# Optimization experiments

Hardware: AMD Instinct MI355X
Metric: run time of the kernel (lower is better)

Reference implementation:

```python
import jax, jax.numpy as jnp
import numpy as np

B, S, IN_F, OUT_F, R = 4, 4096, 4096, 4096, 1024  # new_r = sqrt((4096+4096)*128) = 1024


def setup_inputs() -> dict:
    key = jax.random.key(0)
    kx, kw, kb, ka = jax.random.split(key, 4)
    x = jax.random.normal(kx, (B, S, IN_F), dtype=jnp.float32)
    W = jax.random.normal(kw, (OUT_F, IN_F), dtype=jnp.float32) * 0.02
    b = jax.random.normal(kb, (OUT_F,), dtype=jnp.float32) * 0.02
    A = jax.random.normal(ka, (R, R), dtype=jnp.float32) * 0.02  # lora_A.weight (init zeros in module; randn here to exercise math)
    return {"x": x, "W": W, "b": b, "A": A}


def reference(x, W, b, A):
    # base linear: y = x @ W.T + b
    result = jnp.einsum('bsi,oi->bso', x, W) + b
    # MoRA adapter, mora_type=1, in_f % r == 0 (no padding needed)
    r = A.shape[0]
    sum_inter = IN_F // r  # 4
    in_x = x.reshape(*x.shape[:-1], sum_inter, r).sum(axis=-2)  # [B,S,r]
    out_x = jnp.einsum('bsr,qr->bsq', in_x, A)  # lora_A(in_x): in_x @ A.T
    repeat_time = -(-OUT_F // r)  # ceil = 4
    out_x = jnp.tile(out_x, (1, 1, repeat_time))[..., :OUT_F]
    return result + out_x
```

## Files before the change

### kernel.cpp

```cpp
#include <hip/hip_runtime.h>
#include <hip/hip_bf16.h>
#include <cstdint>


typedef __attribute__((ext_vector_type(8))) short bf16x8;
typedef __attribute__((ext_vector_type(16))) float f32x16;
typedef __attribute__((ext_vector_type(4))) float fvec4;

static constexpr int MTOT = 16384;
static constexpr int KF   = 4096;
static constexpr int NF   = 4096;
static constexpr int BM = 256, BN = 256, BK = 32;
static constexpr int TILE = BM * BK;
static constexpr int KT = KF / BK;
static constexpr int MB = MTOT / BM;
static constexpr int NB = NF / BN;

__global__ __launch_bounds__(256) void tile_x_kernel(const float* __restrict__ x,
                                                     __hip_bfloat16* __restrict__ xt) {
    int blk = blockIdx.x;
    int mb = blk >> 7, kt = blk & 127;
    int tid = threadIdx.x;
    __hip_bfloat16* dst = xt + (size_t)blk * TILE;
#pragma unroll
    for (int it = 0; it < 4; ++it) {
        int e = (it * 256 + tid) * 8;
        int f = e >> 9;
        int l = (e >> 3) & 63;
        int rb = f >> 1, kh = f & 1;
        int row = mb * BM + rb * 32 + (l & 31);
        int k0  = kt * BK + kh * 16 + (l >> 5) * 8;
        const fvec4* s = (const fvec4*)(x + (size_t)row * KF + k0);
        fvec4 v0 = s[0], v1 = s[1];
        union { bf16x8 v; __hip_bfloat16 h[8]; } o;
        o.h[0] = __float2bfloat16(v0[0]); o.h[1] = __float2bfloat16(v0[1]);
        o.h[2] = __float2bfloat16(v0[2]); o.h[3] = __float2bfloat16(v0[3]);
        o.h[4] = __float2bfloat16(v1[0]); o.h[5] = __float2bfloat16(v1[1]);
        o.h[6] = __float2bfloat16(v1[2]); o.h[7] = __float2bfloat16(v1[3]);
        *(bf16x8*)(dst + e) = o.v;
    }
}

__global__ __launch_bounds__(256) void tile_w_kernel(const float* __restrict__ W,
                                                     const float* __restrict__ A,
                                                     __hip_bfloat16* __restrict__ wt) {
    int blk = blockIdx.x;
    int nb = blk >> 7, kt = blk & 127;
    int tid = threadIdx.x;
    __hip_bfloat16* dst = wt + (size_t)blk * TILE;
#pragma unroll
    for (int it = 0; it < 4; ++it) {
        int e = (it * 256 + tid) * 8;
        int f = e >> 9;
        int l = (e >> 3) & 63;
        int rb = f >> 1, kh = f & 1;
        int o  = nb * BN + rb * 32 + (l & 31);
        int k0 = kt * BK + kh * 16 + (l >> 5) * 8;
        const fvec4* sw = (const fvec4*)(W + (size_t)o * KF + k0);
        const fvec4* sa = (const fvec4*)(A + (size_t)(o & 1023) * 1024 + (k0 & 1023));
        fvec4 w0 = sw[0], w1 = sw[1];
        fvec4 a0 = sa[0], a1 = sa[1];
        union { bf16x8 v; __hip_bfloat16 h[8]; } ov;
        ov.h[0] = __float2bfloat16(w0[0] + a0[0]); ov.h[1] = __float2bfloat16(w0[1] + a0[1]);
        ov.h[2] = __float2bfloat16(w0[2] + a0[2]); ov.h[3] = __float2bfloat16(w0[3] + a0[3]);
        ov.h[4] = __float2bfloat16(w1[0] + a1[0]); ov.h[5] = __float2bfloat16(w1[1] + a1[1]);
        ov.h[6] = __float2bfloat16(w1[2] + a1[2]); ov.h[7] = __float2bfloat16(w1[3] + a1[3]);
        *(bf16x8*)(dst + e) = ov.v;
    }
}

__device__ inline void gload_lds16(const __hip_bfloat16* g, __hip_bfloat16* l) {
    __builtin_amdgcn_global_load_lds(
        (const __attribute__((address_space(1))) unsigned int*)g,
        (__attribute__((address_space(3))) unsigned int*)l, 16, 0, 0);
}

#define STG(tt, sl) { const __hip_bfloat16* ga = aP + (size_t)(tt) * TILE;       \
    gload_lds16(ga, As + (sl) * TILE + t8);                                      \
    gload_lds16(ga + 4096, As + (sl) * TILE + 4096 + t8);                        \
    const __hip_bfloat16* gb = bP + (size_t)(tt) * TILE;                         \
    gload_lds16(gb, Bs + (sl) * TILE + t8);                                      \
    gload_lds16(gb + 4096, Bs + (sl) * TILE + 4096 + t8); }

#define RD_KH(P, SL, KH) {                                                       \
    const __hip_bfloat16* ab_ = As + (SL) * TILE + aOff + (KH) * 512;            \
    P##a0 = *(const bf16x8*)(ab_);                                               \
    P##a1 = *(const bf16x8*)(ab_ + 1024);                                        \
    P##a2 = *(const bf16x8*)(ab_ + 2048);                                        \
    P##a3 = *(const bf16x8*)(ab_ + 3072);                                        \
    const __hip_bfloat16* bb_ = Bs + (SL) * TILE + bOff + (KH) * 512;            \
    P##b0 = *(const bf16x8*)(bb_);                                               \
    P##b1 = *(const bf16x8*)(bb_ + 1024); }

#define MM_KH(P) {                                                               \
    acc[0][0] = __builtin_amdgcn_mfma_f32_32x32x16_bf16(P##a0, P##b0, acc[0][0], 0, 0, 0); \
    acc[0][1] = __builtin_amdgcn_mfma_f32_32x32x16_bf16(P##a0, P##b1, acc[0][1], 0, 0, 0); \
    acc[1][0] = __builtin_amdgcn_mfma_f32_32x32x16_bf16(P##a1, P##b0, acc[1][0], 0, 0, 0); \
    acc[1][1] = __builtin_amdgcn_mfma_f32_32x32x16_bf16(P##a1, P##b1, acc[1][1], 0, 0, 0); \
    acc[2][0] = __builtin_amdgcn_mfma_f32_32x32x16_bf16(P##a2, P##b0, acc[2][0], 0, 0, 0); \
    acc[2][1] = __builtin_amdgcn_mfma_f32_32x32x16_bf16(P##a2, P##b1, acc[2][1], 0, 0, 0); \
    acc[3][0] = __builtin_amdgcn_mfma_f32_32x32x16_bf16(P##a3, P##b0, acc[3][0], 0, 0, 0); \
    acc[3][1] = __builtin_amdgcn_mfma_f32_32x32x16_bf16(P##a3, P##b1, acc[3][1], 0, 0, 0); }

#define SGB(m, n) __builtin_amdgcn_sched_group_barrier((m), (n), 0)

#define TILE_STEP(SLT, SLN, STAGE_STMT) {                                        \
    STAGE_STMT;                                                                  \
    RD_KH(B, SLT, 1)                                          \
    MM_KH(A)                                                  \
    RD_KH(A, SLN, 0)                                          \
    MM_KH(B)                                                  \
    SGB(0x30, 2);                                                                \
    SGB(0x100, 1); SGB(0x8, 1); SGB(0x100, 1); SGB(0x8, 1);                      \
    SGB(0x100, 1); SGB(0x8, 1); SGB(0x100, 1); SGB(0x8, 1);                      \
    SGB(0x100, 1); SGB(0x8, 1); SGB(0x100, 1); SGB(0x8, 1);                      \
    SGB(0x30, 2);                                                                \
    SGB(0x8, 2);                                                                 \
    SGB(0x100, 1); SGB(0x8, 1); SGB(0x100, 1); SGB(0x8, 1);                      \
    SGB(0x100, 1); SGB(0x8, 1); SGB(0x100, 1); SGB(0x8, 1);                      \
    SGB(0x100, 1); SGB(0x8, 1); SGB(0x100, 1); SGB(0x8, 1);                      \
    SGB(0x8, 2);                                                                 \
    asm volatile("s_waitcnt vmcnt(4)" ::: "memory");                             \
    __builtin_amdgcn_s_barrier();                                                \
    __builtin_amdgcn_sched_barrier(0);                                           \
    asm volatile("" ::: "memory"); }

__global__ __launch_bounds__(512, 2) void gemm_bf16_kernel(
    const __hip_bfloat16* __restrict__ xt, const __hip_bfloat16* __restrict__ wt,
    const float* __restrict__ bias, float* __restrict__ out) {
    extern __shared__ __hip_bfloat16 lds[];
    __hip_bfloat16* As = lds;
    __hip_bfloat16* Bs = lds + 4 * TILE;

    int bid = blockIdx.x;
    int wg = (bid & 7) * 128 + (bid >> 3);
    int nb = wg >> 6;
    int mb = wg & 63;

    int tid = threadIdx.x;
    int lane = tid & 63;
    int wv = tid >> 6;
    int wm = wv >> 2, wn = wv & 3;
    int t8 = tid * 8;

    int aOff = wm * 4096 + lane * 8;
    int bOff = wn * 2048 + lane * 8;

    const __hip_bfloat16* aP = xt + (size_t)mb * (KT * TILE) + t8;
    const __hip_bfloat16* bP = wt + (size_t)nb * (KT * TILE) + t8;

    f32x16 acc[4][2];
#pragma unroll
    for (int fm = 0; fm < 4; ++fm)
#pragma unroll
        for (int fn = 0; fn < 2; ++fn)
#pragma unroll
            for (int r = 0; r < 16; ++r) acc[fm][fn][r] = 0.f;

    bf16x8 Aa0, Aa1, Aa2, Aa3, Ab0, Ab1;
    bf16x8 Ba0, Ba1, Ba2, Ba3, Bb0, Bb1;

    STG(0, 0); STG(1, 1); STG(2, 2);
    asm volatile("s_waitcnt vmcnt(4)" ::: "memory");
    __builtin_amdgcn_s_barrier();
    asm volatile("" ::: "memory");
    RD_KH(A, 0, 0)

    for (int j = 0; j < KT / 4; ++j) {
        int tb = 4 * j;
        int t4 = tb + 4; if (t4 >= KT) t4 = 0;
        int t5 = tb + 5; if (t5 >= KT) t5 = 0;
        int t6 = tb + 6; if (t6 >= KT) t6 = 0;
        TILE_STEP(0, 1, STG(tb + 3, 3));
        TILE_STEP(1, 2, STG(t4, 0));
        TILE_STEP(2, 3, STG(t5, 1));
        TILE_STEP(3, 0, STG(t6, 2));
    }
    asm volatile("s_waitcnt vmcnt(0)" ::: "memory");

    int row0 = mb * BM + wm * 128;
    int col0 = nb * BN + wn * 64;
    int ln31 = lane & 31;
    int l5 = lane >> 5;
#pragma unroll
    for (int fn = 0; fn < 2; ++fn) {
        int col = col0 + fn * 32 + ln31;
        float bv = bias[col];
#pragma unroll
        for (int fm = 0; fm < 4; ++fm) {
            int rbase = row0 + fm * 32 + 4 * l5;
#pragma unroll
            for (int r = 0; r < 16; ++r) {
                int row = rbase + (r & 3) + 8 * (r >> 2);
                out[(size_t)row * NF + col] = acc[fm][fn][r] + bv;
            }
        }
    }
}

extern "C" void kernel_launch(void* const* d_in, const int* in_sizes, int n_in,
                              void* d_out, int out_size, void* d_ws, size_t ws_size,
                              hipStream_t stream) {
    const float* x = (const float*)d_in[0];
    const float* W = (const float*)d_in[1];
    const float* b = (const float*)d_in[2];
    const float* A = (const float*)d_in[3];
    float* out = (float*)d_out;

    size_t xt_elems = (size_t)MB * KT * TILE;
    size_t wt_elems = (size_t)NB * KT * TILE;
    size_t need = (xt_elems + wt_elems) * sizeof(__hip_bfloat16);
    if (ws_size < need) return;

    __hip_bfloat16* xt = (__hip_bfloat16*)d_ws;
    __hip_bfloat16* wt = xt + xt_elems;

    (void)hipFuncSetAttribute((const void*)gemm_bf16_kernel,
                              hipFuncAttributeMaxDynamicSharedMemorySize, 131072);

    tile_x_kernel<<<MB * KT, 256, 0, stream>>>(x, xt);
    tile_w_kernel<<<NB * KT, 256, 0, stream>>>(W, A, wt);
    gemm_bf16_kernel<<<MB * NB, 512, 131072, stream>>>(xt, wt, b, out);
}
```

Before: 602.7 us.

## Split waves into two instruction schedules to stagger memory and MFMA phases

Waves with wm==0 issue global loads and LDS reads first and then MFMAs, while the other half issue MFMAs first and loads last. The two opposite sched_group_barrier orderings are meant to keep one half of the waves on the matrix cores while the other half uses the memory pipes, in a ping-pong style. This doubles the main-loop code size and adds a wave-uniform branch. It also depends on the compiler honouring the schedule groups, and register pressure may change.

After: 598.8 us. Within noise of the previous version (-0.7%).

```diff
diff --git a/kernel.cpp b/kernel.cpp
--- a/kernel.cpp
+++ b/kernel.cpp
@@ -104,26 +104,43 @@
 
 #define SGB(m, n) __builtin_amdgcn_sched_group_barrier((m), (n), 0)
 
-#define TILE_STEP(SLT, SLN, STAGE_STMT) {                                        \
+#define STEP_END {                                                               \
+    asm volatile("s_waitcnt vmcnt(4)" ::: "memory");                             \
+    __builtin_amdgcn_s_barrier();                                                \
+    __builtin_amdgcn_sched_barrier(0);                                           \
+    asm volatile("" ::: "memory"); }
+
+#define TILE_STEP_R(SLT, SLN, STAGE_STMT) {                                      \
     STAGE_STMT;                                                                  \
     RD_KH(B, SLT, 1)                                          \
     MM_KH(A)                                                  \
     RD_KH(A, SLN, 0)                                          \
     MM_KH(B)                                                  \
-    SGB(0x30, 2);                                                                \
-    SGB(0x100, 1); SGB(0x8, 1); SGB(0x100, 1); SGB(0x8, 1);                      \
-    SGB(0x100, 1); SGB(0x8, 1); SGB(0x100, 1); SGB(0x8, 1);                      \
-    SGB(0x100, 1); SGB(0x8, 1); SGB(0x100, 1); SGB(0x8, 1);                      \
-    SGB(0x30, 2);                                                                \
-    SGB(0x8, 2);                                                                 \
-    SGB(0x100, 1); SGB(0x8, 1); SGB(0x100, 1); SGB(0x8, 1);                      \
-    SGB(0x100, 1); SGB(0x8, 1); SGB(0x100, 1); SGB(0x8, 1);                      \
-    SGB(0x100, 1); SGB(0x8, 1); SGB(0x100, 1); SGB(0x8, 1);                      \
-    SGB(0x8, 2);                                                                 \
-    asm volatile("s_waitcnt vmcnt(4)" ::: "memory");                             \
-    __builtin_amdgcn_s_barrier();                                                \
-    __builtin_amdgcn_sched_barrier(0);                                           \
-    asm volatile("" ::: "memory"); }
+    SGB(0x30, 4);                                                                \
+    SGB(0x100, 1); SGB(0x8, 1); SGB(0x100, 1); SGB(0x8, 1);                      \
+    SGB(0x100, 1); SGB(0x8, 1); SGB(0x100, 1); SGB(0x8, 1);                      \
+    SGB(0x100, 1); SGB(0x8, 1); SGB(0x100, 1); SGB(0x8, 1);                      \
+    SGB(0x100, 1); SGB(0x8, 1); SGB(0x100, 1); SGB(0x8, 1);                      \
+    SGB(0x100, 1); SGB(0x8, 1); SGB(0x100, 1); SGB(0x8, 1);                      \
+    SGB(0x100, 1); SGB(0x8, 1); SGB(0x100, 1); SGB(0x8, 1);                      \
+    SGB(0x8, 4);                                                                 \
+    STEP_END }
+
+#define TILE_STEP_M(SLT, SLN, STAGE_STMT) {                                      \
+    MM_KH(A)                                                  \
+    RD_KH(B, SLT, 1)                                          \
+    MM_KH(B)                                                  \
+    RD_KH(A, SLN, 0)                                          \
+    STAGE_STMT;                                                                  \
+    SGB(0x8, 1); SGB(0x100, 1); SGB(0x8, 1); SGB(0x100, 1);                      \
+    SGB(0x8, 1); SGB(0x100, 1); SGB(0x8, 1); SGB(0x100, 1);                      \
+    SGB(0x8, 1); SGB(0x100, 1); SGB(0x8, 1); SGB(0x100, 1);                      \
+    SGB(0x8, 1); SGB(0x100, 1); SGB(0x8, 1); SGB(0x100, 1);                      \
+    SGB(0x8, 1); SGB(0x100, 1); SGB(0x8, 1); SGB(0x100, 1);                      \
+    SGB(0x8, 1); SGB(0x100, 1); SGB(0x8, 1); SGB(0x100, 1);                      \
+    SGB(0x8, 4);                                                                 \
+    SGB(0x30, 4);                                                                \
+    STEP_END }
 
 __global__ __launch_bounds__(512, 2) void gemm_bf16_kernel(
     const __hip_bfloat16* __restrict__ xt, const __hip_bfloat16* __restrict__ wt,
@@ -166,15 +183,28 @@
     asm volatile("" ::: "memory");
     RD_KH(A, 0, 0)
 
-    for (int j = 0; j < KT / 4; ++j) {
-        int tb = 4 * j;
-        int t4 = tb + 4; if (t4 >= KT) t4 = 0;
-        int t5 = tb + 5; if (t5 >= KT) t5 = 0;
-        int t6 = tb + 6; if (t6 >= KT) t6 = 0;
-        TILE_STEP(0, 1, STG(tb + 3, 3));
-        TILE_STEP(1, 2, STG(t4, 0));
-        TILE_STEP(2, 3, STG(t5, 1));
-        TILE_STEP(3, 0, STG(t6, 2));
+    if (wm == 0) {
+        for (int j = 0; j < KT / 4; ++j) {
+            int tb = 4 * j;
+            int t4 = tb + 4; if (t4 >= KT) t4 = 0;
+            int t5 = tb + 5; if (t5 >= KT) t5 = 0;
+            int t6 = tb + 6; if (t6 >= KT) t6 = 0;
+            TILE_STEP_R(0, 1, STG(tb + 3, 3));
+            TILE_STEP_R(1, 2, STG(t4, 0));
+            TILE_STEP_R(2, 3, STG(t5, 1));
+            TILE_STEP_R(3, 0, STG(t6, 2));
+        }
+    } else {
+        for (int j = 0; j < KT / 4; ++j) {
+            int tb = 4 * j;
+            int t4 = tb + 4; if (t4 >= KT) t4 = 0;
+            int t5 = tb + 5; if (t5 >= KT) t5 = 0;
+            int t6 = tb + 6; if (t6 >= KT) t6 = 0;
+            TILE_STEP_M(0, 1, STG(tb + 3, 3));
+            TILE_STEP_M(1, 2, STG(t4, 0));
+            TILE_STEP_M(2, 3, STG(t5, 1));
+            TILE_STEP_M(3, 0, STG(t6, 2));
+        }
     }
     asm volatile("s_waitcnt vmcnt(0)" ::: "memory");
 
```
